# Kernel tuning notes

Hardware: AMD Instinct MI355X
Metric: run time of the kernel (lower is better)

The kernel has to match this reference:

```python
import jax, jax.numpy as jnp
import numpy as np

N, C, HEADS, NL = 2048, 64, 4, 4
DH = C // HEADS
EPS = 1e-8

def _pdist(pos):
    d2 = jnp.sum((pos[:, None, :] - pos[None, :, :]) ** 2, -1)
    return jnp.sqrt(d2 + 1e-12)

def _edge_weights(pos, adj):
    d = _pdist(pos)
    sigma = jnp.maximum((adj * d).sum() / jnp.maximum(adj.sum(), 1.0), 1e-6)
    return adj * jnp.exp(-(d * d) / (2.0 * sigma * sigma))

def _curvatures(pos, adj):
    deg = jnp.maximum(adj.sum(1), 1.0)
    delta = (adj @ pos) / deg[:, None] - pos          # umbrella Laplacian of coordinates
    H = 0.5 * jnp.linalg.norm(delta, axis=1)          # mean curvature proxy
    d = _pdist(pos)
    r = (adj * d).sum(1) / deg
    var = (adj * (d - r[:, None]) ** 2).sum(1) / deg
    s = jnp.sqrt(var + 1e-12)
    k1, k2 = H + s, H - s
    return dict(mean=H, gaussian=k1 * k2, principal_1=k1, principal_2=k2,
                shape_index=(2.0 / jnp.pi) * jnp.arctan((k1 + k2) / (k1 - k2 + 1e-6)),
                curvedness=jnp.sqrt(0.5 * (k1 ** 2 + k2 ** 2)))

def _ln(x, g, b):
    mu = x.mean(-1, keepdims=True)
    v = ((x - mu) ** 2).mean(-1, keepdims=True)
    return (x - mu) * jax.lax.rsqrt(v + 1e-5) * g + b

def _forward(positions, adj, Wc1, bc1, Wc2, bc2, Win, b_in,
             conv_Wself, conv_bself, conv_Wneigh, conv_bneigh, conv_res,
             diff_W, diff_b, rd_W1, rd_b1, rd_W2, rd_b2, rd_coef,
             ln_g, ln_b, Wq, bq, Wk, bk, Wv, bv, Wo, bo, attn_beta, Wout, bout):
    n = positions.shape[0]
    # --- CurvatureEncoder ---
    cd = _curvatures(positions, adj)
    raw = jnp.stack([cd['mean'], cd['gaussian'], cd['principal_1'],
                     cd['principal_2'], cd['shape_index'], cd['curvedness']], 1)
    raw = (raw - raw.mean(0, keepdims=True)) / jnp.maximum(raw.std(0, ddof=1, keepdims=True), 1e-6)
    curv = jax.nn.silu(raw @ Wc1 + bc1) @ Wc2 + bc2           # (N,16)
    h = jnp.concatenate([positions, curv], -1) @ Win + b_in   # (N,C)
    # --- geometric operators (shared) ---
    W = _edge_weights(positions, adj)
    deg = W.sum(1)
    L = W - jnp.diag(deg)                                     # L = W - D (negative semidefinite)
    Dis = jnp.maximum(deg, EPS) ** -0.5
    L_norm = Dis[:, None] * L * Dis[None, :]
    evals, evecs = jnp.linalg.eigh(L)
    P = W / jnp.maximum(deg, EPS)[:, None]                    # row-stochastic propagation
    t_scales = jnp.array([0.5, 2.0, 8.0], dtype=h.dtype)
    for i in range(NL):
        res = h
        # CotangentConv with learned residual (scale 0.1)
        h = (h @ conv_Wself[i] + conv_bself[i]) \
            + ((P @ h) @ conv_Wneigh[i] + conv_bneigh[i]) \
            + 0.1 * conv_res[i] * h
        h = jax.nn.silu(h)
        if i % 2 == 0:
            # DiffusionConv: 3 heat-kernel scales exp(t*L) via shared eigendecomposition
            j = i // 2
            spec = evecs.T @ h                                # (N,C)
            filt = jnp.exp(t_scales[:, None] * evals[None, :])  # (3,N), evals <= 0
            hd = jnp.einsum('nk,skc->snc', evecs, filt[:, :, None] * spec[None])
            h = h + jnp.einsum('snc,scd->nd', hd, diff_W[j]) + diff_b[j]
        # ReactionDiffusion explicit Euler step (dt = 0.1)
        react = jnp.tanh(h @ rd_W1[i] + rd_b1[i]) @ rd_W2[i] + rd_b2[i]
        h = h + 0.1 * (rd_coef[i] * (L_norm @ h) + react)
        h = _ln(h + res, ln_g[i], ln_b[i])
    # --- CurvatureAttention (adjacency-masked, curvature-biased) ---
    q = (h @ Wq + bq).reshape(n, HEADS, DH)
    k = (h @ Wk + bk).reshape(n, HEADS, DH)
    v = (h @ Wv + bv).reshape(n, HEADS, DH)
    scores = jnp.einsum('nhd,mhd->hnm', q, k) / np.sqrt(DH).astype(np.float32)
    Hc = cd['mean']
    bias = -jax.nn.softplus(attn_beta)[:, None, None] * jnp.abs(Hc[:, None] - Hc[None, :])[None]
    mask = (adj + jnp.eye(n, dtype=adj.dtype)) > 0
    attn = jax.nn.softmax(jnp.where(mask[None], scores + bias, -1e9), -1)
    h = h + jnp.einsum('hnm,mhd->nhd', attn, v).reshape(n, C) @ Wo + bo
    return h @ Wout + bout                                    # (N,1)

def setup_inputs() -> dict:
    key = jax.random.key(0)
    ks = jax.random.split(key, 16)
    pos = jax.random.normal(ks[0], (N, 3), jnp.float32)
    u = jax.random.uniform(ks[1], (N, N))
    m = jnp.triu(u < (16.0 / N), k=1)
    adj = (m | m.T).astype(jnp.float32)           # symmetric 0/1, zero diagonal, avg deg ~16
    def w(k, *s):
        fan = s[-2] if len(s) > 1 else s[-1]
        return jax.random.normal(k, s, jnp.float32) / np.sqrt(fan).astype(np.float32)
    return dict(
        positions=pos, adj=adj,
        Wc1=w(ks[2], 6, 32), bc1=jnp.zeros((32,), jnp.float32),
        Wc2=w(ks[3], 32, 16), bc2=jnp.zeros((16,), jnp.float32),
        Win=w(ks[4], 19, C), b_in=jnp.zeros((C,), jnp.float32),
        conv_Wself=w(ks[5], NL, C, C), conv_bself=jnp.zeros((NL, C), jnp.float32),
        conv_Wneigh=w(ks[6], NL, C, C), conv_bneigh=jnp.zeros((NL, C), jnp.float32),
        conv_res=jnp.ones((NL,), jnp.float32),
        diff_W=w(ks[7], 2, 3, C, C), diff_b=jnp.zeros((2, C), jnp.float32),
        rd_W1=w(ks[8], NL, C, C), rd_b1=jnp.zeros((NL, C), jnp.float32),
        rd_W2=w(ks[9], NL, C, C), rd_b2=jnp.zeros((NL, C), jnp.float32),
        rd_coef=0.5 * jnp.ones((NL, C), jnp.float32),
        ln_g=jnp.ones((NL, C), jnp.float32), ln_b=jnp.zeros((NL, C), jnp.float32),
        Wq=w(ks[10], C, C), bq=jnp.zeros((C,), jnp.float32),
        Wk=w(ks[11], C, C), bk=jnp.zeros((C,), jnp.float32),
        Wv=w(ks[12], C, C), bv=jnp.zeros((C,), jnp.float32),
        Wo=w(ks[13], C, C), bo=jnp.zeros((C,), jnp.float32),
        attn_beta=jnp.ones((HEADS,), jnp.float32),
        Wout=w(ks[14], C, 1), bout=jnp.zeros((1,), jnp.float32),
    )

def reference(positions, adj, Wc1, bc1, Wc2, bc2, Win, b_in,
              conv_Wself, conv_bself, conv_Wneigh, conv_bneigh, conv_res,
              diff_W, diff_b, rd_W1, rd_b1, rd_W2, rd_b2, rd_coef,
              ln_g, ln_b, Wq, bq, Wk, bk, Wv, bv, Wo, bo, attn_beta, Wout, bout):
    return _forward(positions, adj, Wc1, bc1, Wc2, bc2, Win, b_in,
                    conv_Wself, conv_bself, conv_Wneigh, conv_bneigh, conv_res,
                    diff_W, diff_b, rd_W1, rd_b1, rd_W2, rd_b2, rd_coef,
                    ln_g, ln_b, Wq, bq, Wk, bk, Wv, bv, Wo, bo, attn_beta, Wout, bout)
```

## Files before the change

kernel.cpp:

```cpp
#include <hip/hip_runtime.h>
#include <math.h>

#define NPT 2048
#define CH 64
constexpr int TDEG = 14;
constexpr float SCL = 16.0f;


typedef __bf16 bf16_t;
typedef __bf16 bf16x8 __attribute__((ext_vector_type(8)));
typedef __bf16 bf16x4_t __attribute__((ext_vector_type(4)));
typedef float f32x4 __attribute__((ext_vector_type(4)));

__device__ __forceinline__ void gl_lds16(const void* g, void* l) {
  __builtin_amdgcn_global_load_lds(
      (const __attribute__((address_space(1))) void*)g,
      (__attribute__((address_space(3))) void*)l, 16, 0, 0);
}

__global__ __launch_bounds__(256) void pg_geom_csr(
    const float* __restrict__ pos, const float* __restrict__ adj,
    float* __restrict__ raw, float* __restrict__ Hc,
    float* __restrict__ sumA, float* __restrict__ sumAD,
    int* __restrict__ nbr, int* __restrict__ cnt)
{
  __shared__ float sp[NPT * 3];
  __shared__ float red[256 * 6];
  __shared__ int wsum[4];
  int i = blockIdx.x, t = threadIdx.x;
  for (int j = t; j < NPT * 3; j += 256) sp[j] = pos[j];
  __syncthreads();
  float px = sp[3 * i], py = sp[3 * i + 1], pz = sp[3 * i + 2];

  size_t base = (size_t)i * NPT + t * 8;
  float av[8];
  int c = 0;
  for (int u = 0; u < 8; u++) { av[u] = adj[base + u]; c += (av[u] != 0.0f); }
  int sc = c;
  int lane = t & 63;
  for (int off = 1; off < 64; off <<= 1) {
    int v = __shfl_up(sc, off);
    if (lane >= off) sc += v;
  }
  if (lane == 63) wsum[t >> 6] = sc;
  __syncthreads();
  int wprefix = 0;
  for (int w = 0; w < (t >> 6); w++) wprefix += wsum[w];
  int o = wprefix + sc - c;
  int wr = 0;
  for (int u = 0; u < 8; u++)
    if (av[u] != 0.0f) { int p = o + wr; if (p < 64) nbr[i * 64 + p] = t * 8 + u; wr++; }

  float s0 = 0, s1 = 0, s2 = 0, ax = 0, ay = 0, az = 0;
  for (int u = 0; u < 8; u++) {
    if (av[u] != 0.0f) {
      int j = t * 8 + u;
      float dx = sp[3 * j] - px, dy = sp[3 * j + 1] - py, dz = sp[3 * j + 2] - pz;
      float d2 = dx * dx + dy * dy + dz * dz + 1e-12f;
      float d = sqrtf(d2);
      s0 += 1.0f; s1 += d; s2 += d2;
      ax += sp[3 * j]; ay += sp[3 * j + 1]; az += sp[3 * j + 2];
    }
  }
  red[t * 6 + 0] = s0; red[t * 6 + 1] = s1; red[t * 6 + 2] = s2;
  red[t * 6 + 3] = ax; red[t * 6 + 4] = ay; red[t * 6 + 5] = az;
  __syncthreads();
  for (int s = 128; s > 0; s >>= 1) {
    if (t < s)
      for (int q = 0; q < 6; q++) red[t * 6 + q] += red[(t + s) * 6 + q];
    __syncthreads();
  }
  if (t == 0) {
    s0 = red[0]; s1 = red[1]; s2 = red[2]; ax = red[3]; ay = red[4]; az = red[5];
    float degc = fmaxf(s0, 1.0f);
    float dxm = ax / degc - px, dym = ay / degc - py, dzm = az / degc - pz;
    float H = 0.5f * sqrtf(dxm * dxm + dym * dym + dzm * dzm);
    float r = s1 / degc;
    float var = (s2 - 2.0f * r * s1 + r * r * s0) / degc;
    float sdev = sqrtf(var + 1e-12f);
    float k1 = H + sdev, k2 = H - sdev;
    raw[i * 6 + 0] = H;
    raw[i * 6 + 1] = k1 * k2;
    raw[i * 6 + 2] = k1;
    raw[i * 6 + 3] = k2;
    raw[i * 6 + 4] = 0.6366197723675814f * atanf((k1 + k2) / (k1 - k2 + 1e-6f));
    raw[i * 6 + 5] = sqrtf(0.5f * (k1 * k1 + k2 * k2));
    Hc[i] = H;
    sumA[i] = s0; sumAD[i] = s1;
    int tot = wsum[0] + wsum[1] + wsum[2] + wsum[3];
    cnt[i] = min(tot, 64);
  }
}

__global__ __launch_bounds__(256) void pg_stats(
    const float* __restrict__ raw, const float* __restrict__ sumA,
    const float* __restrict__ sumAD, float* __restrict__ stats)
{
  __shared__ float red[256];
  __shared__ float mean6[6];
  int t = threadIdx.x;
  float sa = 0, sad = 0;
  for (int j = t; j < NPT; j += 256) { sa += sumA[j]; sad += sumAD[j]; }
  red[t] = sa; __syncthreads();
  for (int s = 128; s > 0; s >>= 1) { if (t < s) red[t] += red[t + s]; __syncthreads(); }
  float totA = red[0]; __syncthreads();
  red[t] = sad; __syncthreads();
  for (int s = 128; s > 0; s >>= 1) { if (t < s) red[t] += red[t + s]; __syncthreads(); }
  float totAD = red[0]; __syncthreads();
  if (t == 0) {
    float sigma = fmaxf(totAD / fmaxf(totA, 1.0f), 1e-6f);
    stats[0] = 1.0f / (2.0f * sigma * sigma);
    stats[1] = sigma;
  }
  for (int q = 0; q < 6; q++) {
    float s = 0;
    for (int j = t; j < NPT; j += 256) s += raw[j * 6 + q];
    red[t] = s; __syncthreads();
    for (int k = 128; k > 0; k >>= 1) { if (t < k) red[t] += red[t + k]; __syncthreads(); }
    if (t == 0) mean6[q] = red[0] / (float)NPT;
    __syncthreads();
  }
  for (int q = 0; q < 6; q++) {
    float m = mean6[q], s = 0;
    for (int j = t; j < NPT; j += 256) { float d = raw[j * 6 + q] - m; s += d * d; }
    red[t] = s; __syncthreads();
    for (int k = 128; k > 0; k >>= 1) { if (t < k) red[t] += red[t + k]; __syncthreads(); }
    if (t == 0) {
      float sd = sqrtf(red[0] / (float)(NPT - 1));
      stats[2 + q] = m;
      stats[8 + q] = 1.0f / fmaxf(sd, 1e-6f);
    }
    __syncthreads();
  }
}

__global__ __launch_bounds__(64) void pg_wdeg(
    const float* __restrict__ pos, const int* __restrict__ nbr, const int* __restrict__ cnt,
    const float* __restrict__ stats, int2* __restrict__ pack, float* __restrict__ wdeg,
    float* __restrict__ invdeg, float* __restrict__ Dis, float* __restrict__ cvec)
{
  int i = blockIdx.x, t = threadIdx.x;
  int n = cnt[i];
  float inv2s2 = stats[0];
  float px = pos[3 * i], py = pos[3 * i + 1], pz = pos[3 * i + 2];
  float w = 0.0f;
  int j = 0;
  if (t < n) {
    j = nbr[i * 64 + t];
    float dx = pos[3 * j] - px, dy = pos[3 * j + 1] - py, dz = pos[3 * j + 2] - pz;
    float d2 = dx * dx + dy * dy + dz * dz + 1e-12f;
    w = expf(-d2 * inv2s2);
  }
  pack[i * 64 + t] = make_int2(j, __float_as_int(w));
  float s = w;
  for (int off = 1; off < 64; off <<= 1) s += __shfl_xor(s, off);
  if (t == 0) {
    float md = fmaxf(s, 1e-8f);
    wdeg[i] = s;
    invdeg[i] = 1.0f / md;
    float di = 1.0f / sqrtf(md);
    Dis[i] = di;
    cvec[i] = di * di * s;
  }
}

__global__ __launch_bounds__(64) void pg_curv_mlp(
    const float* __restrict__ pos, const float* __restrict__ raw, const float* __restrict__ stats,
    const float* __restrict__ Wc1, const float* __restrict__ bc1,
    const float* __restrict__ Wc2, const float* __restrict__ bc2,
    const float* __restrict__ Win, const float* __restrict__ b_in, float* __restrict__ h)
{
  __shared__ float feat[19];
  __shared__ float nraw[6];
  __shared__ float hid[32];
  int i = blockIdx.x, t = threadIdx.x;
  if (t < 3) feat[t] = pos[3 * i + t];
  if (t < 6) nraw[t] = (raw[i * 6 + t] - stats[2 + t]) * stats[8 + t];
  __syncthreads();
  if (t < 32) {
    float a = bc1[t];
    for (int k = 0; k < 6; k++) a += nraw[k] * Wc1[k * 32 + t];
    hid[t] = a / (1.0f + expf(-a));
  }
  __syncthreads();
  if (t < 16) {
    float a = bc2[t];
    for (int k = 0; k < 32; k++) a += hid[k] * Wc2[k * 16 + t];
    feat[3 + t] = a;
  }
  __syncthreads();
  float a = b_in[t];
  for (int k = 0; k < 19; k++) a += feat[k] * Win[k * CH + t];
  h[i * CH + t] = a;
}

__global__ __launch_bounds__(256) void pg_hinit(
    const int2* __restrict__ pack, const int* __restrict__ cnt,
    const float* __restrict__ wdeg, float* __restrict__ Y)
{
  int r = blockIdx.x, t = threadIdx.x;
  const float c0 = 1.0f / (SCL * (float)TDEG);
  float* row = Y + (size_t)r * NPT;
  for (int j = t * 4; j < NPT; j += 1024)
    *(f32x4*)(row + j) = (f32x4){0.f, 0.f, 0.f, 0.f};
  __syncthreads();
  int n = cnt[r];
  if (t < n) {
    int2 p = pack[r * 64 + t];
    row[p.x] = __int_as_float(p.y) * c0;
  }
  if (t == 0) row[r] = 1.0f - wdeg[r] * c0;
}

template <bool LAST>
__global__ __launch_bounds__(256) void pg_hstep(
    const int2* __restrict__ pack, const int* __restrict__ cnt,
    const float* __restrict__ wdeg, const float* __restrict__ Yin,
    float* __restrict__ Yout, float invc,
    bf16_t* __restrict__ Th, bf16_t* __restrict__ Tl2)
{
  int b = blockIdx.x;
  int s = b & 7, w = b >> 3;
  int t = threadIdx.x;
  int lane = t & 63, v = t >> 6;
  int c0 = s * 256 + lane * 4;
  int r0 = __builtin_amdgcn_readfirstlane(w * 8 + v * 2);
  int r1 = r0 + 1;
  int n0 = cnt[r0], n1 = cnt[r1];
  float wd0 = wdeg[r0], wd1 = wdeg[r1];
  const int2* pr0 = pack + r0 * 64;
  const int2* pr1 = pack + r1 * 64;
  f32x4 y0 = *(const f32x4*)(Yin + (size_t)r0 * NPT + c0);
  f32x4 y1 = *(const f32x4*)(Yin + (size_t)r1 * NPT + c0);
  f32x4 a0, a1, a2, a3, b0, b1, b2, b3;
#pragma unroll
  for (int e = 0; e < 4; e++) {
    a0[e] = -wd0 * y0[e]; b0[e] = -wd1 * y1[e];
    a1[e] = 0.f; a2[e] = 0.f; a3[e] = 0.f;
    b1[e] = 0.f; b2[e] = 0.f; b3[e] = 0.f;
  }
  int nmax = n0 > n1 ? n0 : n1;
  int nn = (nmax + 3) & ~3;
  for (int q = 0; q < nn; q += 4) {
    int2 pa0 = pr0[q], pa1 = pr0[q + 1], pa2 = pr0[q + 2], pa3 = pr0[q + 3];
    int2 pb0 = pr1[q], pb1 = pr1[q + 1], pb2 = pr1[q + 2], pb3 = pr1[q + 3];
    f32x4 ga0 = *(const f32x4*)(Yin + (size_t)pa0.x * NPT + c0);
    f32x4 ga1 = *(const f32x4*)(Yin + (size_t)pa1.x * NPT + c0);
    f32x4 ga2 = *(const f32x4*)(Yin + (size_t)pa2.x * NPT + c0);
    f32x4 ga3 = *(const f32x4*)(Yin + (size_t)pa3.x * NPT + c0);
    f32x4 gb0 = *(const f32x4*)(Yin + (size_t)pb0.x * NPT + c0);
    f32x4 gb1 = *(const f32x4*)(Yin + (size_t)pb1.x * NPT + c0);
    f32x4 gb2 = *(const f32x4*)(Yin + (size_t)pb2.x * NPT + c0);
    f32x4 gb3 = *(const f32x4*)(Yin + (size_t)pb3.x * NPT + c0);
    float wa0 = __int_as_float(pa0.y), wa1 = __int_as_float(pa1.y);
    float wa2 = __int_as_float(pa2.y), wa3 = __int_as_float(pa3.y);
    float wb0 = __int_as_float(pb0.y), wb1 = __int_as_float(pb1.y);
    float wb2 = __int_as_float(pb2.y), wb3 = __int_as_float(pb3.y);
#pragma unroll
    for (int e = 0; e < 4; e++) {
      a0[e] += wa0 * ga0[e]; a1[e] += wa1 * ga1[e];
      a2[e] += wa2 * ga2[e]; a3[e] += wa3 * ga3[e];
      b0[e] += wb0 * gb0[e]; b1[e] += wb1 * gb1[e];
      b2[e] += wb2 * gb2[e]; b3[e] += wb3 * gb3[e];
    }
  }
  f32x4 v0, v1;
#pragma unroll
  for (int e = 0; e < 4; e++) {
    v0[e] = ((c0 + e == r0) ? 1.0f : 0.0f) + ((a0[e] + a1[e]) + (a2[e] + a3[e])) * invc;
    v1[e] = ((c0 + e == r1) ? 1.0f : 0.0f) + ((b0[e] + b1[e]) + (b2[e] + b3[e])) * invc;
  }
  if (LAST) {
    bf16x4_t h0, l0, h1, l1;
#pragma unroll
    for (int e = 0; e < 4; e++) {
      __bf16 hb0 = (__bf16)v0[e];
      __bf16 hb1 = (__bf16)v1[e];
      h0[e] = hb0; l0[e] = (__bf16)(2.0f * (v0[e] - (float)hb0));
      h1[e] = hb1; l1[e] = (__bf16)(2.0f * (v1[e] - (float)hb1));
    }
    *(bf16x4_t*)(Th  + (size_t)r0 * NPT + c0) = h0;
    *(bf16x4_t*)(Tl2 + (size_t)r0 * NPT + c0) = l0;
    *(bf16x4_t*)(Th  + (size_t)r1 * NPT + c0) = h1;
    *(bf16x4_t*)(Tl2 + (size_t)r1 * NPT + c0) = l1;
  } else {
    *(f32x4*)(Yout + (size_t)r0 * NPT + c0) = v0;
    *(f32x4*)(Yout + (size_t)r1 * NPT + c0) = v1;
  }
}

__global__ __launch_bounds__(256) void pg_sq(
    const bf16_t* __restrict__ Ah, const bf16_t* __restrict__ Al2,
    bf16_t* __restrict__ SCh, bf16_t* __restrict__ SCl2)
{
  __shared__ __align__(16) char smem[98304];
  const int t = threadIdx.x;
  const int w = t >> 6, l = t & 63;
  const int lrow = l & 15, lhi = l >> 4;
  int bid = blockIdx.x;
  int sbid = (bid & 7) * 32 + (bid >> 3);
  const int by = sbid >> 4, bx = sbid & 15;
  const int wr = w >> 1, wc = w & 1;

  int offA[4], offB[4];
#pragma unroll
  for (int it = 0; it < 4; it++) {
    int o = it * 4096 + t * 16;
    int r = o >> 7;
    int cb = (o & 127) ^ ((r & 7) << 4);
    offA[it] = (by * 128 + r) * (NPT * 2) + cb;
    offB[it] = (bx * 128 + r) * (NPT * 2) + cb;
  }
  int aoff[4][2], boff[4][2];
#pragma unroll
  for (int m = 0; m < 4; m++) {
    int arow = wr * 64 + m * 16 + lrow;
    int brow = wc * 64 + m * 16 + lrow;
#pragma unroll
    for (int kk = 0; kk < 2; kk++) {
      int kb = kk * 64 + lhi * 16;
      aoff[m][kk] = arow * 128 + (kb ^ ((arow & 7) << 4));
      boff[m][kk] = brow * 128 + (kb ^ ((brow & 7) << 4));
    }
  }

  f32x4 acc[4][4];
#pragma unroll
  for (int m = 0; m < 4; m++)
#pragma unroll
    for (int n = 0; n < 4; n++) acc[m][n] = (f32x4){0.f, 0.f, 0.f, 0.f};

  const int lofs_w = w << 10;
#pragma unroll
  for (int it = 0; it < 4; it++) {
    int lo = it * 4096 + lofs_w;
    gl_lds16((const char*)Ah  + offA[it], smem + lo);
    gl_lds16((const char*)Ah  + offB[it], smem + 16384 + lo);
    gl_lds16((const char*)Al2 + offB[it], smem + 32768 + lo);
  }
  __syncthreads();

  for (int ks = 0; ks < NPT / 64; ks++) {
    if (ks + 1 < NPT / 64) {
      char* nbuf = smem + ((ks + 1) & 1) * 49152;
      size_t kadv = (size_t)(ks + 1) * 128;
#pragma unroll
      for (int it = 0; it < 4; it++) {
        int lo = it * 4096 + lofs_w;
        gl_lds16((const char*)Ah  + offA[it] + kadv, nbuf + lo);
        gl_lds16((const char*)Ah  + offB[it] + kadv, nbuf + 16384 + lo);
        gl_lds16((const char*)Al2 + offB[it] + kadv, nbuf + 32768 + lo);
      }
    }
    const char* cbuf = smem + (ks & 1) * 49152;
#pragma unroll
    for (int kk = 0; kk < 2; kk++) {
      bf16x8 bhf[4], blf[4];
#pragma unroll
      for (int n = 0; n < 4; n++) {
        bhf[n] = *(const bf16x8*)(cbuf + 16384 + boff[n][kk]);
        blf[n] = *(const bf16x8*)(cbuf + 32768 + boff[n][kk]);
      }
#pragma unroll
      for (int m = 0; m < 4; m++) {
        bf16x8 ah = *(const bf16x8*)(cbuf + aoff[m][kk]);
#pragma unroll
        for (int n = 0; n < 4; n++) {
          acc[m][n] = __builtin_amdgcn_mfma_f32_16x16x32_bf16(ah, blf[n], acc[m][n], 0, 0, 0);
          acc[m][n] = __builtin_amdgcn_mfma_f32_16x16x32_bf16(ah, bhf[n], acc[m][n], 0, 0, 0);
        }
      }
    }
    __syncthreads();
  }

  const int gr0 = by * 128 + wr * 64 + lhi * 4;
  const int gc0 = bx * 128 + wc * 64 + lrow;
#pragma unroll
  for (int m = 0; m < 4; m++) {
#pragma unroll
    for (int n = 0; n < 4; n++) {
      int gc = gc0 + n * 16;
#pragma unroll
      for (int r = 0; r < 4; r++) {
        float c = acc[m][n][r];
        __bf16 hb = (__bf16)c;
        size_t o = (size_t)(gr0 + m * 16 + r) * NPT + gc;
        SCh[o] = hb;
        SCl2[o] = (__bf16)(2.0f * (c - (float)hb));
      }
    }
  }
}

__global__ __launch_bounds__(256) void pg_fix(
    const bf16_t* __restrict__ Sh, const bf16_t* __restrict__ Sl2,
    bf16_t* __restrict__ Oh, bf16_t* __restrict__ Ol2)
{
  __shared__ float T2[128][129];
  int bj = blockIdx.x, bi = blockIdx.y;
  int t = threadIdx.x;
  int row = t >> 1, cb = (t & 1) * 64;
  size_t base2 = ((size_t)(bj * 128 + row)) * NPT + bi * 128 + cb;
  for (int i = 0; i < 8; i++) {
    bf16x8 h8 = *(const bf16x8*)(Sh + base2 + i * 8);
    bf16x8 l8 = *(const bf16x8*)(Sl2 + base2 + i * 8);
#pragma unroll
    for (int e = 0; e < 8; e++)
      T2[row][cb + i * 8 + e] = (float)h8[e] + 0.5f * (float)l8[e];
  }
  __syncthreads();
  size_t base1 = ((size_t)(bi * 128 + row)) * NPT + bj * 128 + cb;
  for (int i = 0; i < 8; i++) {
    bf16x8 h8 = *(const bf16x8*)(Sh + base1 + i * 8);
    bf16x8 l8 = *(const bf16x8*)(Sl2 + base1 + i * 8);
    bf16x8 oh, ol;
#pragma unroll
    for (int e = 0; e < 8; e++) {
      float s1 = (float)h8[e] + 0.5f * (float)l8[e];
      float s2 = T2[cb + i * 8 + e][row];
      float cv = 0.5f * (s1 + s2);
      __bf16 hb = (__bf16)cv;
      oh[e] = hb;
      ol[e] = (__bf16)(2.0f * (cv - (float)hb));
    }
    *(bf16x8*)(Oh + base1 + i * 8) = oh;
    *(bf16x8*)(Ol2 + base1 + i * 8) = ol;
  }
}

__global__ __launch_bounds__(256) void pg_splitx(
    const float* __restrict__ X, bf16_t* __restrict__ XTh,
    bf16_t* __restrict__ XTl, bf16_t* __restrict__ XTh2)
{
  __shared__ float sX[64][65];
  int t = threadIdx.x;
  int r0 = blockIdx.x * 64;
  for (int u = 0; u < 16; u++) {
    int idx = u * 256 + t;
    int r = idx >> 6, c = idx & 63;
    sX[r][c] = X[(size_t)(r0 + r) * CH + c];
  }
  __syncthreads();
  int c = t >> 6;
  int rr = t & 63;
  for (int cc = c; cc < 64; cc += 4) {
    float v = sX[rr][cc];
    __bf16 hb = (__bf16)v;
    XTh[(size_t)cc * NPT + r0 + rr] = hb;
    XTl[(size_t)cc * NPT + r0 + rr] = (__bf16)(v - (float)hb);
    XTh2[(size_t)cc * NPT + r0 + rr] = (__bf16)(0.5f * (float)hb);
  }
}

__global__ __launch_bounds__(256) void pg_emm(
    const bf16_t* __restrict__ E05h, const bf16_t* __restrict__ E05l,
    const bf16_t* __restrict__ E2h,  const bf16_t* __restrict__ E2l,
    const bf16_t* __restrict__ E8h,  const bf16_t* __restrict__ E8l,
    const bf16_t* __restrict__ XTh,  const bf16_t* __restrict__ XTl,
    const bf16_t* __restrict__ XTh2, float* __restrict__ hd)
{
  __shared__ __align__(16) char smem[81920];
  const int t = threadIdx.x;
  const int w = t >> 6, l = t & 63;
  const int lrow = l & 15, lhi = l >> 4;
  const int scale = blockIdx.y;
  const bf16_t* Eh = (scale == 0) ? E05h : (scale == 1) ? E2h : E8h;
  const bf16_t* El = (scale == 0) ? E05l : (scale == 1) ? E2l : E8l;
  const int rb = blockIdx.x;

  int offA[2], offB[2];
#pragma unroll
  for (int it = 0; it < 2; it++) {
    int o = it * 4096 + t * 16;
    int r = o >> 7;
    int cb = (o & 127) ^ ((r & 7) << 4);
    offA[it] = (rb * 64 + r) * (NPT * 2) + cb;
    offB[it] = r * (NPT * 2) + cb;
  }
  int aoff[2], boff[4][2];
  {
    int arow = w * 16 + lrow;
#pragma unroll
    for (int kk = 0; kk < 2; kk++) {
      int kb = kk * 64 + lhi * 16;
      aoff[kk] = arow * 128 + (kb ^ ((arow & 7) << 4));
    }
  }
#pragma unroll
  for (int n = 0; n < 4; n++) {
    int brow = n * 16 + lrow;
#pragma unroll
    for (int kk = 0; kk < 2; kk++) {
      int kb = kk * 64 + lhi * 16;
      boff[n][kk] = brow * 128 + (kb ^ ((brow & 7) << 4));
    }
  }

  f32x4 acc[4];
#pragma unroll
  for (int n = 0; n < 4; n++) acc[n] = (f32x4){0.f, 0.f, 0.f, 0.f};

  const int lofs_w = w << 10;
#pragma unroll
  for (int it = 0; it < 2; it++) {
    int lo = it * 4096 + lofs_w;
    gl_lds16((const char*)Eh   + offA[it], smem + lo);
    gl_lds16((const char*)El   + offA[it], smem + 8192 + lo);
    gl_lds16((const char*)XTh  + offB[it], smem + 16384 + lo);
    gl_lds16((const char*)XTl  + offB[it], smem + 24576 + lo);
    gl_lds16((const char*)XTh2 + offB[it], smem + 32768 + lo);
  }
  __syncthreads();

  for (int ks = 0; ks < NPT / 64; ks++) {
    if (ks + 1 < NPT / 64) {
      char* nbuf = smem + ((ks + 1) & 1) * 40960;
      size_t kadv = (size_t)(ks + 1) * 128;
#pragma unroll
      for (int it = 0; it < 2; it++) {
        int lo = it * 4096 + lofs_w;
        gl_lds16((const char*)Eh   + offA[it] + kadv, nbuf + lo);
        gl_lds16((const char*)El   + offA[it] + kadv, nbuf + 8192 + lo);
        gl_lds16((const char*)XTh  + offB[it] + kadv, nbuf + 16384 + lo);
        gl_lds16((const char*)XTl  + offB[it] + kadv, nbuf + 24576 + lo);
        gl_lds16((const char*)XTh2 + offB[it] + kadv, nbuf + 32768 + lo);
      }
    }
    const char* cbuf = smem + (ks & 1) * 40960;
#pragma unroll
    for (int kk = 0; kk < 2; kk++) {
      bf16x8 eh  = *(const bf16x8*)(cbuf + aoff[kk]);
      bf16x8 el2 = *(const bf16x8*)(cbuf + 8192 + aoff[kk]);
#pragma unroll
      for (int n = 0; n < 4; n++) {
        bf16x8 xh  = *(const bf16x8*)(cbuf + 16384 + boff[n][kk]);
        bf16x8 xl  = *(const bf16x8*)(cbuf + 24576 + boff[n][kk]);
        bf16x8 xh2 = *(const bf16x8*)(cbuf + 32768 + boff[n][kk]);
        acc[n] = __builtin_amdgcn_mfma_f32_16x16x32_bf16(el2, xh2, acc[n], 0, 0, 0);
        acc[n] = __builtin_amdgcn_mfma_f32_16x16x32_bf16(eh, xl, acc[n], 0, 0, 0);
        acc[n] = __builtin_amdgcn_mfma_f32_16x16x32_bf16(eh, xh, acc[n], 0, 0, 0);
      }
    }
    __syncthreads();
  }

  float* Y = hd + (size_t)scale * NPT * CH;
  const int gr0 = rb * 64 + w * 16 + lhi * 4;
#pragma unroll
  for (int n = 0; n < 4; n++) {
    int gc = n * 16 + lrow;
#pragma unroll
    for (int r = 0; r < 4; r++)
      Y[(size_t)(gr0 + r) * CH + gc] = acc[n][r];
  }
}

__global__ __launch_bounds__(64) void pg_convP(
    const int2* __restrict__ pack, const int* __restrict__ cnt,
    const float* __restrict__ invdeg, const float* __restrict__ h,
    const float* __restrict__ Ws, const float* __restrict__ bs,
    const float* __restrict__ Wn, const float* __restrict__ bn,
    const float* __restrict__ cres, float* __restrict__ out)
{
  __shared__ float sh[64], sp2[64];
  int i = blockIdx.x, t = threadIdx.x;
  sh[t] = h[i * CH + t];
  int n = cnt[i];
  float acc = 0.0f;
  for (int q = 0; q < n; q++) {
    int2 p = pack[i * 64 + q];
    acc += __int_as_float(p.y) * h[(size_t)p.x * CH + t];
  }
  sp2[t] = acc * invdeg[i];
  __syncthreads();
  float a = bs[t] + bn[t] + 0.1f * cres[0] * sh[t];
  for (int k = 0; k < 64; k++) a += sh[k] * Ws[k * CH + t] + sp2[k] * Wn[k * CH + t];
  out[i * CH + t] = a / (1.0f + expf(-a));
}

__global__ __launch_bounds__(64) void pg_difffuse(
    const float* __restrict__ h2, const float* __restrict__ hd,
    const float* __restrict__ dW, const float* __restrict__ db, float* __restrict__ out)
{
  __shared__ float sh[3][64];
  int i = blockIdx.x, t = threadIdx.x;
  for (int s = 0; s < 3; s++) sh[s][t] = hd[(size_t)s * NPT * CH + i * CH + t];
  __syncthreads();
  float a = h2[i * CH + t] + db[t];
  for (int s = 0; s < 3; s++) {
    const float* w = dW + s * CH * CH;
    for (int k = 0; k < 64; k++) a += sh[s][k] * w[k * CH + t];
  }
  out[i * CH + t] = a;
}

__global__ __launch_bounds__(64) void pg_tlr(
    const int2* __restrict__ pack, const int* __restrict__ cnt,
    const float* __restrict__ Dis, const float* __restrict__ cvec,
    const float* __restrict__ h3,
    const float* __restrict__ W1, const float* __restrict__ b1,
    const float* __restrict__ W2, const float* __restrict__ b2,
    const float* __restrict__ rdc,
    const float* __restrict__ g, const float* __restrict__ b,
    float* __restrict__ hio)
{
  __shared__ float sh[64], st[64];
  int i = blockIdx.x, t = threadIdx.x;
  sh[t] = h3[i * CH + t];
  __syncthreads();
  float a = b1[t];
  for (int k = 0; k < 64; k++) a += sh[k] * W1[k * CH + t];
  st[t] = tanhf(a);
  int n = cnt[i];
  float accL = 0.0f;
  for (int q = 0; q < n; q++) {
    int2 p = pack[i * 64 + q];
    accL += __int_as_float(p.y) * Dis[p.x] * h3[(size_t)p.x * CH + t];
  }
  float tLv = accL * Dis[i] - cvec[i] * sh[t];
  __syncthreads();
  float react = b2[t];
  for (int k = 0; k < 64; k++) react += st[k] * W2[k * CH + t];
  float x = sh[t] + 0.1f * (rdc[t] * tLv + react) + hio[i * CH + t];
  float s = x;
  for (int off = 1; off < 64; off <<= 1) s += __shfl_xor(s, off);
  float mu = s * (1.0f / 64.0f);
  float d = x - mu;
  float v = d * d;
  for (int off = 1; off < 64; off <<= 1) v += __shfl_xor(v, off);
  v *= (1.0f / 64.0f);
  hio[i * CH + t] = d * (1.0f / sqrtf(v + 1e-5f)) * g[t] + b[t];
}

__global__ __launch_bounds__(64) void pg_qkv(
    const float* __restrict__ h,
    const float* __restrict__ Wq, const float* __restrict__ bq,
    const float* __restrict__ Wk, const float* __restrict__ bk,
    const float* __restrict__ Wv, const float* __restrict__ bv,
    float* __restrict__ q, float* __restrict__ kb, float* __restrict__ vb)
{
  __shared__ float sh[64];
  int i = blockIdx.x, t = threadIdx.x;
  sh[t] = h[i * CH + t];
  __syncthreads();
  float aq = bq[t], ak = bk[t], avv = bv[t];
  for (int k = 0; k < 64; k++) {
    float x = sh[k];
    aq += x * Wq[k * CH + t];
    ak += x * Wk[k * CH + t];
    avv += x * Wv[k * CH + t];
  }
  q[i * CH + t] = aq;
  kb[i * CH + t] = ak;
  vb[i * CH + t] = avv;
}

__global__ __launch_bounds__(256) void pg_attn_out(
    const float* __restrict__ q, const float* __restrict__ kb, const float* __restrict__ vb,
    const int* __restrict__ nbr, const int* __restrict__ cnt,
    const float* __restrict__ Hc, const float* __restrict__ beta,
    const float* __restrict__ h,
    const float* __restrict__ Wo, const float* __restrict__ bo,
    const float* __restrict__ Wout, const float* __restrict__ bout,
    float* __restrict__ out)
{
  __shared__ float av_s[64];
  int i = blockIdx.x;
  int t = threadIdx.x;
  int head = t >> 6, lane = t & 63;
  float sp_b = logf(1.0f + expf(beta[head]));
  float hci = Hc[i];
  const float* qp = q + i * CH + head * 16;
  float qr[16];
#pragma unroll
  for (int d = 0; d < 16; d++) qr[d] = qp[d];
  int n = cnt[i];
  int K = n + 1;
  float mx = -1e30f, den = 0.0f;
  float vac[16];
#pragma unroll
  for (int d = 0; d < 16; d++) vac[d] = 0.0f;
  for (int m = lane; m < K; m += 64) {
    int j = (m == n) ? i : nbr[i * 64 + m];
    const float* kp = kb + (size_t)j * CH + head * 16;
    float sc = 0.0f;
#pragma unroll
    for (int d = 0; d < 16; d++) sc += qr[d] * kp[d];
    sc *= 0.25f;
    sc -= sp_b * fabsf(hci - Hc[j]);
    float nm = fmaxf(mx, sc);
    float corr = expf(mx - nm);
    float p = expf(sc - nm);
    den = den * corr + p;
    const float* vp = vb + (size_t)j * CH + head * 16;
#pragma unroll
    for (int d = 0; d < 16; d++) vac[d] = vac[d] * corr + p * vp[d];
    mx = nm;
  }
  for (int off = 32; off > 0; off >>= 1) {
    float omx = __shfl_down(mx, off);
    float oden = __shfl_down(den, off);
    float ov[16];
#pragma unroll
    for (int d = 0; d < 16; d++) ov[d] = __shfl_down(vac[d], off);
    float nm = fmaxf(mx, omx);
    float c1 = expf(mx - nm), c2 = expf(omx - nm);
    den = den * c1 + oden * c2;
#pragma unroll
    for (int d = 0; d < 16; d++) vac[d] = vac[d] * c1 + ov[d] * c2;
    mx = nm;
  }
  if (lane == 0) {
    float inv = 1.0f / den;
    for (int d = 0; d < 16; d++) av_s[head * 16 + d] = vac[d] * inv;
  }
  __syncthreads();
  if (t < 64) {
    float a = h[i * CH + t] + bo[t];
    for (int k = 0; k < 64; k++) a += av_s[k] * Wo[k * CH + t];
    float s = a * Wout[t];
    for (int off = 1; off < 64; off <<= 1) s += __shfl_xor(s, off);
    if (t == 0) out[i] = s + bout[0];
  }
}

extern "C" void kernel_launch(void* const* d_in, const int* in_sizes, int n_in,
                              void* d_out, int out_size, void* d_ws, size_t ws_size,
                              hipStream_t stream)
{
  const float* pos   = (const float*)d_in[0];
  const float* adj   = (const float*)d_in[1];
  const float* Wc1   = (const float*)d_in[2];
  const float* bc1   = (const float*)d_in[3];
  const float* Wc2   = (const float*)d_in[4];
  const float* bc2   = (const float*)d_in[5];
  const float* Win   = (const float*)d_in[6];
  const float* b_in  = (const float*)d_in[7];
  const float* cWs   = (const float*)d_in[8];
  const float* cbs   = (const float*)d_in[9];
  const float* cWn   = (const float*)d_in[10];
  const float* cbn   = (const float*)d_in[11];
  const float* cres  = (const float*)d_in[12];
  const float* dW    = (const float*)d_in[13];
  const float* db    = (const float*)d_in[14];
  const float* rW1   = (const float*)d_in[15];
  const float* rb1   = (const float*)d_in[16];
  const float* rW2   = (const float*)d_in[17];
  const float* rb2   = (const float*)d_in[18];
  const float* rdc   = (const float*)d_in[19];
  const float* lng   = (const float*)d_in[20];
  const float* lnb   = (const float*)d_in[21];
  const float* Wq    = (const float*)d_in[22];
  const float* bq    = (const float*)d_in[23];
  const float* Wk    = (const float*)d_in[24];
  const float* bk    = (const float*)d_in[25];
  const float* Wv    = (const float*)d_in[26];
  const float* bv    = (const float*)d_in[27];
  const float* Wo    = (const float*)d_in[28];
  const float* bo    = (const float*)d_in[29];
  const float* abeta = (const float*)d_in[30];
  const float* Wout  = (const float*)d_in[31];
  const float* bout  = (const float*)d_in[32];

  const size_t NNe = (size_t)NPT * NPT;
  const size_t NC  = (size_t)NPT * CH;
  const size_t P   = NNe * 2;

  char* base = (char*)d_ws;
  bf16_t* E05h = (bf16_t*)(base + 0 * P);
  bf16_t* E05l = (bf16_t*)(base + 1 * P);
  bf16_t* E2h  = (bf16_t*)(base + 2 * P);
  bf16_t* E2l  = (bf16_t*)(base + 3 * P);
  bf16_t* E8h  = (bf16_t*)(base + 4 * P);
  bf16_t* E8l  = (bf16_t*)(base + 5 * P);
  bf16_t* SAh  = (bf16_t*)(base + 6 * P);
  bf16_t* SAl  = (bf16_t*)(base + 7 * P);
  bf16_t* SBh  = (bf16_t*)(base + 8 * P);
  bf16_t* SBl  = (bf16_t*)(base + 9 * P);
  float*  M0   = (float*)(base + 0 * P);
  float*  M1   = (float*)(base + 2 * P);
  bf16_t* XTh  = (bf16_t*)(base + 12 * P);
  bf16_t* XTl  = (bf16_t*)(base + 12 * P + (size_t)NPT * CH * 2);
  bf16_t* XTh2 = (bf16_t*)(base + 12 * P + (size_t)NPT * CH * 4);
  float*  smb  = (float*)(base + 12 * P + 1024 * 1024);

  float* h   = smb;
  float* tA  = h + NC;
  float* tB  = tA + NC;
  float* hd  = tB + NC;
  float* q   = hd + 3 * NC;
  float* kbf = q + NC;
  float* vbf = kbf + NC;
  float* raw = vbf + NC;
  float* sm  = raw + 8 * NPT;
  float* sumA   = sm;
  float* sumAD  = sm + NPT;
  float* wdeg   = sm + 2 * NPT;
  float* invdeg = sm + 3 * NPT;
  float* Dis    = sm + 4 * NPT;
  float* cvec   = sm + 5 * NPT;
  float* Hc     = sm + 6 * NPT;
  float* stats  = sm + 7 * NPT;
  int*   nbr    = (int*)(sm + 8 * NPT);
  int*   cnt    = nbr + (size_t)NPT * 64;
  int2*  pack   = (int2*)(cnt + NPT);

  size_t need = 12 * P + 1024 * 1024
              + (9 * NC + 16 * (size_t)NPT) * 4
              + (size_t)NPT * 64 * 4 + NPT * 4 + (size_t)NPT * 64 * 8 + 256;
  if (ws_size < need) return;

  pg_geom_csr<<<NPT, 256, 0, stream>>>(pos, adj, raw, Hc, sumA, sumAD, nbr, cnt);
  pg_stats<<<1, 256, 0, stream>>>(raw, sumA, sumAD, stats);
  pg_wdeg<<<NPT, 64, 0, stream>>>(pos, nbr, cnt, stats, pack, wdeg, invdeg, Dis, cvec);
  pg_curv_mlp<<<NPT, 64, 0, stream>>>(pos, raw, stats, Wc1, bc1, Wc2, bc2, Win, b_in, h);

  pg_hinit<<<NPT, 256, 0, stream>>>(pack, cnt, wdeg, M0);
  float* cur = M0;
  float* nxt = M1;
  for (int k = TDEG - 1; k >= 2; k--) {
    pg_hstep<false><<<NPT, 256, 0, stream>>>(pack, cnt, wdeg, cur, nxt,
                                             1.0f / (SCL * (float)k), nullptr, nullptr);
    float* tmp = cur; cur = nxt; nxt = tmp;
  }
  pg_hstep<true><<<NPT, 256, 0, stream>>>(pack, cnt, wdeg, cur, nullptr,
                                          1.0f / SCL, SAh, SAl);

  dim3 gfix(16, 16);
  pg_sq <<<256, 256, 0, stream>>>(SAh, SAl, E05h, E05l);
  pg_fix<<<gfix, 256, 0, stream>>>(E05h, E05l, SBh, SBl);
  pg_sq <<<256, 256, 0, stream>>>(SBh, SBl, E05h, E05l);
  pg_fix<<<gfix, 256, 0, stream>>>(E05h, E05l, SAh, SAl);
  pg_sq <<<256, 256, 0, stream>>>(SAh, SAl, SBh, SBl);
  pg_fix<<<gfix, 256, 0, stream>>>(SBh, SBl, E05h, E05l);
  pg_sq <<<256, 256, 0, stream>>>(E05h, E05l, E2h, E2l);
  pg_fix<<<gfix, 256, 0, stream>>>(E2h, E2l, SBh, SBl);
  pg_sq <<<256, 256, 0, stream>>>(SBh, SBl, SAh, SAl);
  pg_fix<<<gfix, 256, 0, stream>>>(SAh, SAl, E2h, E2l);
  pg_sq <<<256, 256, 0, stream>>>(E2h, E2l, SBh, SBl);
  pg_fix<<<gfix, 256, 0, stream>>>(SBh, SBl, SAh, SAl);
  pg_sq <<<256, 256, 0, stream>>>(SAh, SAl, SBh, SBl);
  pg_fix<<<gfix, 256, 0, stream>>>(SBh, SBl, E8h, E8l);

  for (int i = 0; i < 4; i++) {
    pg_convP<<<NPT, 64, 0, stream>>>(pack, cnt, invdeg, h,
                                     cWs + i * 4096, cbs + i * 64,
                                     cWn + i * 4096, cbn + i * 64, cres + i, tA);
    float* h3 = tA;
    if ((i & 1) == 0) {
      int j = i >> 1;
      pg_splitx<<<32, 256, 0, stream>>>(tA, XTh, XTl, XTh2);
      pg_emm<<<dim3(32, 3), 256, 0, stream>>>(E05h, E05l, E2h, E2l, E8h, E8l,
                                              XTh, XTl, XTh2, hd);
      pg_difffuse<<<NPT, 64, 0, stream>>>(tA, hd, dW + j * 3 * 4096, db + j * 64, tB);
      h3 = tB;
    }
    pg_tlr<<<NPT, 64, 0, stream>>>(pack, cnt, Dis, cvec, h3,
                                   rW1 + i * 4096, rb1 + i * 64,
                                   rW2 + i * 4096, rb2 + i * 64,
                                   rdc + i * 64, lng + i * 64, lnb + i * 64, h);
  }

  pg_qkv<<<NPT, 64, 0, stream>>>(h, Wq, bq, Wk, bk, Wv, bv, q, kbf, vbf);
  pg_attn_out<<<NPT, 256, 0, stream>>>(q, kbf, vbf, nbr, cnt, Hc, abeta,
                                       h, Wo, bo, Wout, bout, (float*)d_out);
}
```

Baseline: 841.4 us.

## Replace dense E8 squaring chain with repeated E2 applications to features

Stops forming the E8 heat kernel by extra dense matrix squarings. Instead it applies E2 four times to the 64-channel feature matrix (E8 = E2^4), chaining matrix-vector-block products that re-split their output into hi/lo bf16 transposed buffers in the epilogue. It also drops the intermediate fix steps in the E0.5 squaring chain. This trades several 2048^3 squaring GEMMs for extra skinny GEMMs with only 32 blocks each, and accumulates error differently across the chained products.

New measurement: 897.5 us. +6.7%, slower.

```diff
diff --git a/kernel.cpp b/kernel.cpp
--- a/kernel.cpp
+++ b/kernel.cpp
@@ -453,20 +453,18 @@
   }
 }
 
-__global__ __launch_bounds__(256) void pg_emm(
-    const bf16_t* __restrict__ E05h, const bf16_t* __restrict__ E05l,
-    const bf16_t* __restrict__ E2h,  const bf16_t* __restrict__ E2l,
-    const bf16_t* __restrict__ E8h,  const bf16_t* __restrict__ E8l,
-    const bf16_t* __restrict__ XTh,  const bf16_t* __restrict__ XTl,
-    const bf16_t* __restrict__ XTh2, float* __restrict__ hd)
+template <int MODE>
+__global__ __launch_bounds__(256) void pg_emm1(
+    const bf16_t* __restrict__ Eh, const bf16_t* __restrict__ El2,
+    const bf16_t* __restrict__ XTh, const bf16_t* __restrict__ XTl,
+    const bf16_t* __restrict__ XTh2,
+    float* __restrict__ Y,
+    bf16_t* __restrict__ OTh, bf16_t* __restrict__ OTl, bf16_t* __restrict__ OTh2)
 {
   __shared__ __align__(16) char smem[81920];
   const int t = threadIdx.x;
   const int w = t >> 6, l = t & 63;
   const int lrow = l & 15, lhi = l >> 4;
-  const int scale = blockIdx.y;
-  const bf16_t* Eh = (scale == 0) ? E05h : (scale == 1) ? E2h : E8h;
-  const bf16_t* El = (scale == 0) ? E05l : (scale == 1) ? E2l : E8l;
   const int rb = blockIdx.x;
 
   int offA[2], offB[2];
@@ -506,7 +504,7 @@
   for (int it = 0; it < 2; it++) {
     int lo = it * 4096 + lofs_w;
     gl_lds16((const char*)Eh   + offA[it], smem + lo);
-    gl_lds16((const char*)El   + offA[it], smem + 8192 + lo);
+    gl_lds16((const char*)El2  + offA[it], smem + 8192 + lo);
     gl_lds16((const char*)XTh  + offB[it], smem + 16384 + lo);
     gl_lds16((const char*)XTl  + offB[it], smem + 24576 + lo);
     gl_lds16((const char*)XTh2 + offB[it], smem + 32768 + lo);
@@ -521,7 +519,7 @@
       for (int it = 0; it < 2; it++) {
         int lo = it * 4096 + lofs_w;
         gl_lds16((const char*)Eh   + offA[it] + kadv, nbuf + lo);
-        gl_lds16((const char*)El   + offA[it] + kadv, nbuf + 8192 + lo);
+        gl_lds16((const char*)El2  + offA[it] + kadv, nbuf + 8192 + lo);
         gl_lds16((const char*)XTh  + offB[it] + kadv, nbuf + 16384 + lo);
         gl_lds16((const char*)XTl  + offB[it] + kadv, nbuf + 24576 + lo);
         gl_lds16((const char*)XTh2 + offB[it] + kadv, nbuf + 32768 + lo);
@@ -545,14 +543,43 @@
     __syncthreads();
   }
 
-  float* Y = hd + (size_t)scale * NPT * CH;
-  const int gr0 = rb * 64 + w * 16 + lhi * 4;
-#pragma unroll
-  for (int n = 0; n < 4; n++) {
-    int gc = n * 16 + lrow;
-#pragma unroll
-    for (int r = 0; r < 4; r++)
-      Y[(size_t)(gr0 + r) * CH + gc] = acc[n][r];
+  const int lr0 = w * 16 + lhi * 4;
+  if (MODE & 1) {
+#pragma unroll
+    for (int n = 0; n < 4; n++) {
+      int gc = n * 16 + lrow;
+#pragma unroll
+      for (int r = 0; r < 4; r++)
+        Y[(size_t)(rb * 64 + lr0 + r) * CH + gc] = acc[n][r];
+    }
+  }
+  if (MODE & 2) {
+    float* S = (float*)smem;
+#pragma unroll
+    for (int n = 0; n < 4; n++) {
+      int gc = n * 16 + lrow;
+#pragma unroll
+      for (int r = 0; r < 4; r++)
+        S[(lr0 + r) * 65 + gc] = acc[n][r];
+    }
+    __syncthreads();
+    int c = t & 63, rc = (t >> 6) * 16;
+    bf16x8 oh[2], ol[2], oh2[2];
+#pragma unroll
+    for (int half = 0; half < 2; half++) {
+#pragma unroll
+      for (int e = 0; e < 8; e++) {
+        float v = S[(rc + half * 8 + e) * 65 + c];
+        __bf16 hb = (__bf16)v;
+        oh[half][e] = hb;
+        ol[half][e] = (__bf16)(v - (float)hb);
+        oh2[half][e] = (__bf16)(0.5f * (float)hb);
+      }
+    }
+    size_t ob = (size_t)c * NPT + rb * 64 + rc;
+    *(bf16x8*)(OTh + ob) = oh[0];  *(bf16x8*)(OTh + ob + 8) = oh[1];
+    *(bf16x8*)(OTl + ob) = ol[0];  *(bf16x8*)(OTl + ob + 8) = ol[1];
+    *(bf16x8*)(OTh2 + ob) = oh2[0]; *(bf16x8*)(OTh2 + ob + 8) = oh2[1];
   }
 }
 
@@ -766,24 +793,26 @@
   const size_t NNe = (size_t)NPT * NPT;
   const size_t NC  = (size_t)NPT * CH;
   const size_t P   = NNe * 2;
+  const size_t XP  = (size_t)NPT * CH * 2;
 
   char* base = (char*)d_ws;
   bf16_t* E05h = (bf16_t*)(base + 0 * P);
   bf16_t* E05l = (bf16_t*)(base + 1 * P);
   bf16_t* E2h  = (bf16_t*)(base + 2 * P);
   bf16_t* E2l  = (bf16_t*)(base + 3 * P);
-  bf16_t* E8h  = (bf16_t*)(base + 4 * P);
-  bf16_t* E8l  = (bf16_t*)(base + 5 * P);
-  bf16_t* SAh  = (bf16_t*)(base + 6 * P);
-  bf16_t* SAl  = (bf16_t*)(base + 7 * P);
-  bf16_t* SBh  = (bf16_t*)(base + 8 * P);
-  bf16_t* SBl  = (bf16_t*)(base + 9 * P);
+  bf16_t* SAh  = (bf16_t*)(base + 4 * P);
+  bf16_t* SAl  = (bf16_t*)(base + 5 * P);
+  bf16_t* SBh  = (bf16_t*)(base + 6 * P);
+  bf16_t* SBl  = (bf16_t*)(base + 7 * P);
   float*  M0   = (float*)(base + 0 * P);
   float*  M1   = (float*)(base + 2 * P);
-  bf16_t* XTh  = (bf16_t*)(base + 12 * P);
-  bf16_t* XTl  = (bf16_t*)(base + 12 * P + (size_t)NPT * CH * 2);
-  bf16_t* XTh2 = (bf16_t*)(base + 12 * P + (size_t)NPT * CH * 4);
-  float*  smb  = (float*)(base + 12 * P + 1024 * 1024);
+  bf16_t* XT0h  = (bf16_t*)(base + 8 * P);
+  bf16_t* XT0l  = (bf16_t*)(base + 8 * P + 1 * XP);
+  bf16_t* XT0h2 = (bf16_t*)(base + 8 * P + 2 * XP);
+  bf16_t* XT1h  = (bf16_t*)(base + 8 * P + 3 * XP);
+  bf16_t* XT1l  = (bf16_t*)(base + 8 * P + 4 * XP);
+  bf16_t* XT1h2 = (bf16_t*)(base + 8 * P + 5 * XP);
+  float*  smb  = (float*)(base + 8 * P + 2 * 1024 * 1024);
 
   float* h   = smb;
   float* tA  = h + NC;
@@ -806,7 +835,7 @@
   int*   cnt    = nbr + (size_t)NPT * 64;
   int2*  pack   = (int2*)(cnt + NPT);
 
-  size_t need = 12 * P + 1024 * 1024
+  size_t need = 8 * P + 2 * 1024 * 1024
               + (9 * NC + 16 * (size_t)NPT) * 4
               + (size_t)NPT * 64 * 4 + NPT * 4 + (size_t)NPT * 64 * 8 + 256;
   if (ws_size < need) return;
@@ -828,20 +857,13 @@
                                           1.0f / SCL, SAh, SAl);
 
   dim3 gfix(16, 16);
-  pg_sq <<<256, 256, 0, stream>>>(SAh, SAl, E05h, E05l);
-  pg_fix<<<gfix, 256, 0, stream>>>(E05h, E05l, SBh, SBl);
-  pg_sq <<<256, 256, 0, stream>>>(SBh, SBl, E05h, E05l);
-  pg_fix<<<gfix, 256, 0, stream>>>(E05h, E05l, SAh, SAl);
+  pg_sq <<<256, 256, 0, stream>>>(SAh, SAl, SBh, SBl);
+  pg_sq <<<256, 256, 0, stream>>>(SBh, SBl, SAh, SAl);
   pg_sq <<<256, 256, 0, stream>>>(SAh, SAl, SBh, SBl);
   pg_fix<<<gfix, 256, 0, stream>>>(SBh, SBl, E05h, E05l);
-  pg_sq <<<256, 256, 0, stream>>>(E05h, E05l, E2h, E2l);
-  pg_fix<<<gfix, 256, 0, stream>>>(E2h, E2l, SBh, SBl);
-  pg_sq <<<256, 256, 0, stream>>>(SBh, SBl, SAh, SAl);
-  pg_fix<<<gfix, 256, 0, stream>>>(SAh, SAl, E2h, E2l);
-  pg_sq <<<256, 256, 0, stream>>>(E2h, E2l, SBh, SBl);
-  pg_fix<<<gfix, 256, 0, stream>>>(SBh, SBl, SAh, SAl);
+  pg_sq <<<256, 256, 0, stream>>>(E05h, E05l, SAh, SAl);
   pg_sq <<<256, 256, 0, stream>>>(SAh, SAl, SBh, SBl);
-  pg_fix<<<gfix, 256, 0, stream>>>(SBh, SBl, E8h, E8l);
+  pg_fix<<<gfix, 256, 0, stream>>>(SBh, SBl, E2h, E2l);
 
   for (int i = 0; i < 4; i++) {
     pg_convP<<<NPT, 64, 0, stream>>>(pack, cnt, invdeg, h,
@@ -850,9 +872,17 @@
     float* h3 = tA;
     if ((i & 1) == 0) {
       int j = i >> 1;
-      pg_splitx<<<32, 256, 0, stream>>>(tA, XTh, XTl, XTh2);
-      pg_emm<<<dim3(32, 3), 256, 0, stream>>>(E05h, E05l, E2h, E2l, E8h, E8l,
-                                              XTh, XTl, XTh2, hd);
+      pg_splitx<<<32, 256, 0, stream>>>(tA, XT0h, XT0l, XT0h2);
+      pg_emm1<1><<<32, 256, 0, stream>>>(E05h, E05l, XT0h, XT0l, XT0h2,
+                                         hd, nullptr, nullptr, nullptr);
+      pg_emm1<3><<<32, 256, 0, stream>>>(E2h, E2l, XT0h, XT0l, XT0h2,
+                                         hd + NC, XT1h, XT1l, XT1h2);
+      pg_emm1<2><<<32, 256, 0, stream>>>(E2h, E2l, XT1h, XT1l, XT1h2,
+                                         nullptr, XT0h, XT0l, XT0h2);
+      pg_emm1<2><<<32, 256, 0, stream>>>(E2h, E2l, XT0h, XT0l, XT0h2,
+                                         nullptr, XT1h, XT1l, XT1h2);
+      pg_emm1<1><<<32, 256, 0, stream>>>(E2h, E2l, XT1h, XT1l, XT1h2,
+                                         hd + 2 * NC, nullptr, nullptr, nullptr);
       pg_difffuse<<<NPT, 64, 0, stream>>>(tA, hd, dW + j * 3 * 4096, db + j * 64, tB);
       h3 = tB;
     }
```
